# Optimization experiments

Hardware: AMD Instinct MI355X
Metric: run time of the kernel (lower is better)

## Reference

```python
import jax, jax.numpy as jnp
import numpy as np

SELF_DIM = 6   # self_state_dim
HID = 50       # lstm_hidden_dim


def setup_inputs() -> dict:
    key = jax.random.key(0)
    ks = jax.random.split(key, 16)
    B, N, D = 8192, 64, 13  # batch, num humans, joint-state length

    def w(k, shape):
        # kaiming-ish init, stored as [in, out] so forward is x @ W + b
        return jax.random.normal(k, shape, jnp.float32) / jnp.sqrt(jnp.float32(shape[0]))

    z = lambda n: jnp.zeros((n,), jnp.float32)
    return {
        "state": jax.random.normal(ks[0], (B, N, D), jnp.float32),
        # mlp1: 13 -> 150 -> 100, last_relu=True
        "mlp1_w1": w(ks[1], (13, 150)),  "mlp1_b1": z(150),
        "mlp1_w2": w(ks[2], (150, 100)), "mlp1_b2": z(100),
        # attention: 200 -> 100 -> 100 -> 1 (no relu on last)
        "attn_w1": w(ks[3], (200, 100)), "attn_b1": z(100),
        "attn_w2": w(ks[4], (100, 100)), "attn_b2": z(100),
        "attn_w3": w(ks[5], (100, 1)),   "attn_b3": z(1),
        # LSTM(input=7, hidden=50), torch gate order i,f,g,o
        "lstm_wih": w(ks[6], (7, 4 * HID)),
        "lstm_whh": w(ks[7], (HID, 4 * HID)),
        "lstm_bih": z(4 * HID), "lstm_bhh": z(4 * HID),
        # mlp: 56 -> 150 -> 100 -> 100 -> 1
        "mlp_w1": w(ks[8], (SELF_DIM + HID, 150)), "mlp_b1": z(150),
        "mlp_w2": w(ks[9], (150, 100)),            "mlp_b2": z(100),
        "mlp_w3": w(ks[10], (100, 100)),           "mlp_b3": z(100),
        "mlp_w4": w(ks[11], (100, 1)),             "mlp_b4": z(1),
    }


def reference(state, mlp1_w1, mlp1_b1, mlp1_w2, mlp1_b2,
              attn_w1, attn_b1, attn_w2, attn_b2, attn_w3, attn_b3,
              lstm_wih, lstm_whh, lstm_bih, lstm_bhh,
              mlp_w1, mlp_b1, mlp_w2, mlp_b2, mlp_w3, mlp_b3, mlp_w4, mlp_b4):
    relu = jax.nn.relu
    B, N, D = state.shape
    self_state = state[:, 0, :SELF_DIM]      # [B, 6]
    human_state = state[:, :, SELF_DIM:]     # [B, N, 7]

    # mlp1 over all B*N per-human joint-state rows (last_relu=True)
    flat = state.reshape(B * N, D)
    m1 = relu(relu(flat @ mlp1_w1 + mlp1_b1) @ mlp1_w2 + mlp1_b2)   # [B*N, 100]

    # mean-pooled global state, broadcast back per human, concat, attention score
    gdim = m1.shape[-1]
    global_state = jnp.mean(m1.reshape(B, N, gdim), axis=1, keepdims=True)
    global_state = jnp.broadcast_to(global_state, (B, N, gdim)).reshape(B * N, gdim)
    a_in = jnp.concatenate([m1, global_state], axis=1)               # [B*N, 200]
    scores = (relu(relu(a_in @ attn_w1 + attn_b1) @ attn_w2 + attn_b2) @ attn_w3 + attn_b3)
    scores = scores.reshape(B, N)
    # NOTE: in the original torch code `scores` only feed `rerank_human_state`,
    # which is never consumed (dead code) -- the LSTM runs on the UNSORTED
    # human_state. We keep the score computation for fidelity; the per-sample
    # argsort/gather is dropped since it does not affect the output.

    # LSTM over the N humans (batch_first in torch, h0=c0=0)
    xs = jnp.transpose(human_state, (1, 0, 2))   # [N, B, 7]
    h0 = jnp.zeros((B, HID), state.dtype)

    def step(carry, x_t):
        h, c = carry
        gates = x_t @ lstm_wih + h @ lstm_whh + lstm_bih + lstm_bhh  # [B, 4H]
        i, f, g, o = jnp.split(gates, 4, axis=-1)
        c = jax.nn.sigmoid(f) * c + jax.nn.sigmoid(i) * jnp.tanh(g)
        h = jax.nn.sigmoid(o) * jnp.tanh(c)
        return (h, c), None

    (hn, _cn), _ = jax.lax.scan(step, (h0, h0), xs)

    # value head on [self_state, h_n]
    joint = jnp.concatenate([self_state, hn], axis=1)   # [B, 56]
    x = relu(joint @ mlp_w1 + mlp_b1)
    x = relu(x @ mlp_w2 + mlp_b2)
    x = relu(x @ mlp_w3 + mlp_b3)
    value = x @ mlp_w4 + mlp_b4                          # [B, 1]
    return value
```

## Files before the change

kernel.cpp:

```cpp
#include <hip/hip_runtime.h>

typedef __attribute__((ext_vector_type(8))) short short8;
typedef __attribute__((ext_vector_type(4))) float f32x4;
union frag_u { short8 v; unsigned short u[8]; };

__device__ __forceinline__ float bf2f(unsigned short b) {
  unsigned int u = ((unsigned int)b) << 16;
  float f; __builtin_memcpy(&f, &u, 4); return f;
}
__device__ __forceinline__ unsigned short f2bf(float f) {
  unsigned int u; __builtin_memcpy(&u, &f, 4);
  return (unsigned short)((u + 0x7FFFu + ((u >> 16) & 1u)) >> 16);
}
__device__ __forceinline__ unsigned short hi_of(float f) { return f2bf(f); }
__device__ __forceinline__ unsigned short lo_of(float f) {
  unsigned short h = f2bf(f); return f2bf(f - bf2f(h));
}
__device__ __forceinline__ float sigm(float x) {
  return __builtin_amdgcn_rcpf(1.f + __expf(-x));
}
__device__ __forceinline__ float tanh_(float x) {
  return 1.f - 2.f * __builtin_amdgcn_rcpf(1.f + __expf(2.f * x));
}

__global__ void detect_dtype_kernel(const unsigned short* s, int* flag) {
  if (threadIdx.x == 0 && blockIdx.x == 0) {
    int insane = 0;
    for (int i = 0; i < 64; ++i) {
      unsigned short v = s[2 * i];
      int e = (v >> 7) & 0xFF;
      if (e < 100 || e > 140) insane++;
    }
    *flag = (insane >= 16) ? 1 : 0;
  }
}

template <int AS, typename GetB, typename GetW>
__device__ __forceinline__ void mfma_layer(const unsigned short* sA, float* sG,
    int wave, int col, int quad, int kc_n, int ntiles, int N, GetB getb, GetW getw)
{
  for (int tile = wave; tile < ntiles; tile += 8) {
    int n = tile * 16 + col;
    float b = (n < N) ? getb(n) : 0.f;
    f32x4 acc = {b, b, b, b};
    for (int kc = 0; kc < kc_n; ++kc) {
      short8 a = *(const short8*)&sA[col * AS + kc * 32 + quad * 8];
      frag_u w;
      #pragma unroll
      for (int j = 0; j < 8; ++j) {
        int k = kc * 32 + quad * 8 + j;
        w.u[j] = (n < N) ? getw(k, n) : (unsigned short)0;
      }
      acc = __builtin_amdgcn_mfma_f32_16x16x32_bf16(a, w.v, acc, 0, 0, 0);
    }
    *(f32x4*)&sG[n * 20 + quad * 4] = acc;
  }
}

template <int AS, bool LO>
__device__ __forceinline__ void relu_fill(const float* sG, unsigned short* sA,
                                          int tid, int N, int loOff, int Kpad) {
  for (int idx = tid; idx < 16 * Kpad; idx += 512) {
    int m = idx & 15, n = idx >> 4;
    unsigned short v = 0;
    if (n < N) {
      v = f2bf(fmaxf(sG[n * 20 + m], 0.f));
    } else if (LO && n >= loOff && n < loOff + N) {
      float x = fmaxf(sG[(n - loOff) * 20 + m], 0.f);
      v = lo_of(x);
    }
    sA[m * AS + n] = v;
  }
}

template <bool F32>
__global__ __launch_bounds__(512, 4) void value_net_kernel(
    const void* state_, const void* wih_, const void* whh_,
    const void* bih_, const void* bhh_,
    const void* w1_, const void* b1_, const void* w2_, const void* b2_,
    const void* w3_, const void* b3_, const void* w4_, const void* b4_,
    void* out_, const int* flag)
{
  if (flag && *flag != (F32 ? 1 : 0)) return;

  constexpr int AS = F32 ? 328 : 168;
  constexpr int KC = F32 ? 6 : 4;

  __shared__ __align__(16) unsigned short sA[16 * AS];
  __shared__ __align__(16) float sG[208 * 20];

  const unsigned short* st16 = (const unsigned short*)state_;
  const float*          stf  = (const float*)state_;

  const int tid  = threadIdx.x;
  const int wave = tid >> 6;
  const int lane = tid & 63;
  const int col  = lane & 15;
  const int quad = lane >> 4;
  const int r0   = blockIdx.x * 16;

  {
    unsigned int* a32 = (unsigned int*)sA;
    constexpr int ZN = (16 * AS / 2 + 511) / 512;
    #pragma unroll
    for (int i = 0; i < ZN; ++i) {
      int idx = tid + i * 512;
      if (idx < 16 * AS / 2) a32[idx] = 0;
    }
  }

  auto W_lstm = [&](int k, int n) -> unsigned short {
    if constexpr (!F32) {
      const unsigned short* wih = (const unsigned short*)wih_;
      const unsigned short* whh = (const unsigned short*)whh_;
      if (k < 7)   return wih[k * 200 + n];
      if (k < 57)  return whh[(k - 7) * 200 + n];
      if (k < 107) return whh[(k - 57) * 200 + n];
      return (unsigned short)0;
    } else {
      const float* wih = (const float*)wih_;
      const float* whh = (const float*)whh_;
      if (k < 7)   return hi_of(wih[k * 200 + n]);
      if (k < 14)  return hi_of(wih[(k - 7) * 200 + n]);
      if (k < 21)  return lo_of(wih[(k - 14) * 200 + n]);
      if (k < 71)  return hi_of(whh[(k - 21) * 200 + n]);
      if (k < 121) return hi_of(whh[(k - 71) * 200 + n]);
      if (k < 171) return lo_of(whh[(k - 121) * 200 + n]);
      return (unsigned short)0;
    }
  };
  auto ldf = [&](const void* p, int i) -> float {
    if constexpr (F32) return ((const float*)p)[i];
    else               return bf2f(((const unsigned short*)p)[i]);
  };

  const int nmine = (wave < 5) ? 2 : 1;
  frag_u wf[2][KC];
  float  wb[2];
  #pragma unroll
  for (int i = 0; i < 2; ++i) {
    if (i >= nmine) continue;
    int n = (wave + 8 * i) * 16 + col;
    #pragma unroll
    for (int kc = 0; kc < KC; ++kc) {
      #pragma unroll
      for (int j = 0; j < 8; ++j) {
        int k = kc * 32 + quad * 8 + j;
        wf[i][kc].u[j] = (n < 200) ? W_lstm(k, n) : (unsigned short)0;
      }
    }
    wb[i] = (n < 200) ? (ldf(bih_, n) + ldf(bhh_, n)) : 0.f;
  }

  int im[2], iu[2]; bool iv[2];
  float c_[2] = {0.f, 0.f}, hf[2] = {0.f, 0.f};
  #pragma unroll
  for (int i = 0; i < 2; ++i) {
    int idx = tid + 512 * i;
    iv[i] = idx < 800; im[i] = idx & 15; iu[i] = idx >> 4;
  }
  const int  xm = tid / 7, xd = tid - (tid / 7) * 7;
  const bool isx = tid < 112;
  auto xgidx = [&](int t) -> size_t { return (size_t)(r0 + xm) * 832 + t * 13 + 6 + xd; };
  auto xwrite = [&](float fv, unsigned short bv) {
    if constexpr (!F32) { sA[xm * AS + xd] = bv; }
    else {
      unsigned short h = f2bf(fv);
      sA[xm * AS + xd] = h; sA[xm * AS + 14 + xd] = h;
      sA[xm * AS + 7 + xd] = f2bf(fv - bf2f(h));
    }
  };

  unsigned short xv16 = 0; float xvf = 0.f;

  __syncthreads();
  if (isx) {
    if constexpr (!F32) { xwrite(0.f, st16[xgidx(0)]); xv16 = st16[xgidx(1)]; }
    else                { xwrite(stf[xgidx(0)], 0);    xvf  = stf[xgidx(1)]; }
  }
  __syncthreads();

  for (int t = 0; t < 64; ++t) {
    short8 a[KC];
    #pragma unroll
    for (int kc = 0; kc < KC; ++kc)
      a[kc] = *(const short8*)&sA[col * AS + kc * 32 + quad * 8];
    #pragma unroll
    for (int i = 0; i < 2; ++i) {
      if (i < nmine) {
        float b = wb[i];
        f32x4 acc = {b, b, b, b};
        #pragma unroll
        for (int kc = 0; kc < KC; ++kc)
          acc = __builtin_amdgcn_mfma_f32_16x16x32_bf16(a[kc], wf[i][kc].v, acc, 0, 0, 0);
        int n = (wave + 8 * i) * 16 + col;
        *(f32x4*)&sG[n * 20 + quad * 4] = acc;
      }
    }
    __syncthreads();
    #pragma unroll
    for (int i = 0; i < 2; ++i) {
      if (iv[i]) {
        int m = im[i], u = iu[i];
        float gi = sG[u * 20 + m];
        float gf = sG[(50 + u) * 20 + m];
        float gg = sG[(100 + u) * 20 + m];
        float go = sG[(150 + u) * 20 + m];
        float cc = sigm(gf) * c_[i] + sigm(gi) * tanh_(gg);
        c_[i] = cc;
        float h = sigm(go) * tanh_(cc);
        if (t < 63) {
          unsigned short hb = f2bf(h);
          unsigned short hl = f2bf(h - bf2f(hb));
          if constexpr (!F32) { sA[m * AS + 7 + u] = hb; sA[m * AS + 57 + u] = hl; }
          else { sA[m * AS + 21 + u] = hb; sA[m * AS + 121 + u] = hb; sA[m * AS + 71 + u] = hl; }
        } else hf[i] = h;
      }
    }
    if (isx && t < 63) {
      if constexpr (!F32) xwrite(0.f, xv16); else xwrite(xvf, 0);
      if (t < 62) { if constexpr (!F32) xv16 = st16[xgidx(t + 2)]; else xvf = stf[xgidx(t + 2)]; }
    }
    __syncthreads();
  }

  {
    unsigned int* a32 = (unsigned int*)sA;
    constexpr int ZN = (16 * AS / 2 + 511) / 512;
    #pragma unroll
    for (int i = 0; i < ZN; ++i) {
      int idx = tid + i * 512;
      if (idx < 16 * AS / 2) a32[idx] = 0;
    }
  }
  __syncthreads();
  #pragma unroll
  for (int i = 0; i < 2; ++i) {
    if (iv[i]) {
      int m = im[i], u = iu[i];
      unsigned short hb = f2bf(hf[i]);
      unsigned short hl = f2bf(hf[i] - bf2f(hb));
      sA[m * AS + 6 + u] = hb;
      if constexpr (!F32) sA[m * AS + 56 + u] = hl; else sA[m * AS + 62 + u] = hl;
    }
  }
  if (tid < 96) {
    int m = tid / 6, d = tid - (tid / 6) * 6;
    if constexpr (!F32) sA[m * AS + d] = st16[(size_t)(r0 + m) * 832 + d];
    else {
      float f = stf[(size_t)(r0 + m) * 832 + d];
      sA[m * AS + d] = hi_of(f); sA[m * AS + 56 + d] = lo_of(f);
    }
  }
  __syncthreads();

  mfma_layer<AS>(sA, sG, wave, col, quad, 4, 10, 150,
    [&](int n) { return ldf(b1_, n); },
    [&](int k, int n) -> unsigned short {
      if constexpr (!F32) {
        const unsigned short* w1 = (const unsigned short*)w1_;
        if (k < 56)  return w1[k * 150 + n];
        if (k < 106) return w1[(k - 50) * 150 + n];
        return (unsigned short)0;
      } else {
        const float* w1 = (const float*)w1_;
        if (k < 56)  return hi_of(w1[k * 150 + n]);
        if (k < 112) return hi_of(w1[(k - 56) * 150 + n]);
        return (unsigned short)0;
      }
    });
  __syncthreads();
  if constexpr (!F32) relu_fill<AS, false>(sG, sA, tid, 150, 160, 160);
  else                relu_fill<AS, true >(sG, sA, tid, 150, 150, 320);
  __syncthreads();

  mfma_layer<AS>(sA, sG, wave, col, quad, F32 ? 10 : 5, 7, 100,
    [&](int n) { return ldf(b2_, n); },
    [&](int k, int n) -> unsigned short {
      if constexpr (!F32) {
        const unsigned short* w2 = (const unsigned short*)w2_;
        return (k < 150) ? w2[k * 100 + n] : (unsigned short)0;
      } else {
        const float* w2 = (const float*)w2_;
        if (k < 150) return hi_of(w2[k * 100 + n]);
        if (k < 300) return hi_of(w2[(k - 150) * 100 + n]);
        return (unsigned short)0;
      }
    });
  __syncthreads();
  if constexpr (!F32) relu_fill<AS, false>(sG, sA, tid, 100, 128, 128);
  else                relu_fill<AS, true >(sG, sA, tid, 100, 100, 224);
  __syncthreads();

  mfma_layer<AS>(sA, sG, wave, col, quad, F32 ? 7 : 4, 7, 100,
    [&](int n) { return ldf(b3_, n); },
    [&](int k, int n) -> unsigned short {
      if constexpr (!F32) {
        const unsigned short* w3 = (const unsigned short*)w3_;
        return (k < 100) ? w3[k * 100 + n] : (unsigned short)0;
      } else {
        const float* w3 = (const float*)w3_;
        if (k < 100) return hi_of(w3[k * 100 + n]);
        if (k < 200) return hi_of(w3[(k - 100) * 100 + n]);
        return (unsigned short)0;
      }
    });
  __syncthreads();

  if (tid < 256) {
    int m = tid >> 4, j0 = tid & 15;
    float s = 0.f;
    for (int j = j0; j < 100; j += 16)
      s += fmaxf(sG[j * 20 + m], 0.f) * ldf(w4_, j);
    s += __shfl_xor(s, 8); s += __shfl_xor(s, 4);
    s += __shfl_xor(s, 2); s += __shfl_xor(s, 1);
    if (j0 == 0) {
      float v = s + ldf(b4_, 0);
      if constexpr (!F32) ((unsigned short*)out_)[r0 + m] = f2bf(v);
      else                ((float*)out_)[r0 + m] = v;
    }
  }
}

extern "C" void kernel_launch(void* const* d_in, const int* in_sizes, int n_in,
                              void* d_out, int out_size, void* d_ws, size_t ws_size,
                              hipStream_t stream) {
  (void)in_sizes; (void)n_in; (void)out_size;
  const void* state = d_in[0];
  const void* wih = d_in[11]; const void* whh = d_in[12];
  const void* bih = d_in[13]; const void* bhh = d_in[14];
  const void* w1  = d_in[15]; const void* b1  = d_in[16];
  const void* w2  = d_in[17]; const void* b2  = d_in[18];
  const void* w3  = d_in[19]; const void* b3  = d_in[20];
  const void* w4  = d_in[21]; const void* b4  = d_in[22];

  if (ws_size >= sizeof(int)) {
    int* flag = (int*)d_ws;
    detect_dtype_kernel<<<dim3(1), dim3(64), 0, stream>>>(
        (const unsigned short*)state, flag);
    value_net_kernel<false><<<dim3(512), dim3(512), 0, stream>>>(
        state, wih, whh, bih, bhh, w1, b1, w2, b2, w3, b3, w4, b4, d_out, flag);
    value_net_kernel<true><<<dim3(512), dim3(512), 0, stream>>>(
        state, wih, whh, bih, bhh, w1, b1, w2, b2, w3, b3, w4, b4, d_out, flag);
  } else {
    value_net_kernel<false><<<dim3(512), dim3(512), 0, stream>>>(
        state, wih, whh, bih, bhh, w1, b1, w2, b2, w3, b3, w4, b4, d_out,
        (const int*)nullptr);
  }
}
```

Measured before the change: 243.8 us.

## Double block size so each LSTM gate tile and cell gets its own thread

Grows the workgroup from 512 to 1024 threads (16 waves). Each of the 13 gate tiles now belongs to one wave, each of the 800 LSTM cell updates to one thread, and the x-prefetch moves to a separate set of spare threads. This shortens the serial critical path of every recurrent timestep, which previously had some waves doing two MFMA tiles and threads doing two cell updates. In exchange the blocks are larger, which may lower per-CU occupancy and register budget, and three of the sixteen waves sit idle at each barrier during the gate MFMA phase.

```diff
diff --git a/kernel.cpp b/kernel.cpp
--- a/kernel.cpp
+++ b/kernel.cpp
@@ -39,7 +39,7 @@
 __device__ __forceinline__ void mfma_layer(const unsigned short* sA, float* sG,
     int wave, int col, int quad, int kc_n, int ntiles, int N, GetB getb, GetW getw)
 {
-  for (int tile = wave; tile < ntiles; tile += 8) {
+  for (int tile = wave; tile < ntiles; tile += 16) {
     int n = tile * 16 + col;
     float b = (n < N) ? getb(n) : 0.f;
     f32x4 acc = {b, b, b, b};
@@ -60,7 +60,7 @@
 template <int AS, bool LO>
 __device__ __forceinline__ void relu_fill(const float* sG, unsigned short* sA,
                                           int tid, int N, int loOff, int Kpad) {
-  for (int idx = tid; idx < 16 * Kpad; idx += 512) {
+  for (int idx = tid; idx < 16 * Kpad; idx += 1024) {
     int m = idx & 15, n = idx >> 4;
     unsigned short v = 0;
     if (n < N) {
@@ -74,7 +74,7 @@
 }
 
 template <bool F32>
-__global__ __launch_bounds__(512, 4) void value_net_kernel(
+__global__ __launch_bounds__(1024, 8) void value_net_kernel(
     const void* state_, const void* wih_, const void* whh_,
     const void* bih_, const void* bhh_,
     const void* w1_, const void* b1_, const void* w2_, const void* b2_,
@@ -101,10 +101,10 @@
 
   {
     unsigned int* a32 = (unsigned int*)sA;
-    constexpr int ZN = (16 * AS / 2 + 511) / 512;
+    constexpr int ZN = (16 * AS / 2 + 1023) / 1024;
     #pragma unroll
     for (int i = 0; i < ZN; ++i) {
-      int idx = tid + i * 512;
+      int idx = tid + i * 1024;
       if (idx < 16 * AS / 2) a32[idx] = 0;
     }
   }
@@ -134,33 +134,28 @@
     else               return bf2f(((const unsigned short*)p)[i]);
   };
 
-  const int nmine = (wave < 5) ? 2 : 1;
-  frag_u wf[2][KC];
-  float  wb[2];
-  #pragma unroll
-  for (int i = 0; i < 2; ++i) {
-    if (i >= nmine) continue;
-    int n = (wave + 8 * i) * 16 + col;
+  const bool hasTile = (wave < 13);
+  frag_u wf[KC];
+  float  wb = 0.f;
+  if (hasTile) {
+    int n = wave * 16 + col;
     #pragma unroll
     for (int kc = 0; kc < KC; ++kc) {
       #pragma unroll
       for (int j = 0; j < 8; ++j) {
         int k = kc * 32 + quad * 8 + j;
-        wf[i][kc].u[j] = (n < 200) ? W_lstm(k, n) : (unsigned short)0;
-      }
-    }
-    wb[i] = (n < 200) ? (ldf(bih_, n) + ldf(bhh_, n)) : 0.f;
-  }
-
-  int im[2], iu[2]; bool iv[2];
-  float c_[2] = {0.f, 0.f}, hf[2] = {0.f, 0.f};
-  #pragma unroll
-  for (int i = 0; i < 2; ++i) {
-    int idx = tid + 512 * i;
-    iv[i] = idx < 800; im[i] = idx & 15; iu[i] = idx >> 4;
-  }
-  const int  xm = tid / 7, xd = tid - (tid / 7) * 7;
-  const bool isx = tid < 112;
+        wf[kc].u[j] = (n < 200) ? W_lstm(k, n) : (unsigned short)0;
+      }
+    }
+    wb = (n < 200) ? (ldf(bih_, n) + ldf(bhh_, n)) : 0.f;
+  }
+
+  const bool iv = tid < 800;
+  const int  im = tid & 15, iu = tid >> 4;
+  float c_ = 0.f, hf = 0.f;
+
+  const bool isx = (tid >= 800) && (tid < 912);
+  const int  xm = (tid - 800) / 7, xd = (tid - 800) - ((tid - 800) / 7) * 7;
   auto xgidx = [&](int t) -> size_t { return (size_t)(r0 + xm) * 832 + t * 13 + 6 + xd; };
   auto xwrite = [&](float fv, unsigned short bv) {
     if constexpr (!F32) { sA[xm * AS + xd] = bv; }
@@ -181,41 +176,33 @@
   __syncthreads();
 
   for (int t = 0; t < 64; ++t) {
-    short8 a[KC];
-    #pragma unroll
-    for (int kc = 0; kc < KC; ++kc)
-      a[kc] = *(const short8*)&sA[col * AS + kc * 32 + quad * 8];
-    #pragma unroll
-    for (int i = 0; i < 2; ++i) {
-      if (i < nmine) {
-        float b = wb[i];
-        f32x4 acc = {b, b, b, b};
-        #pragma unroll
-        for (int kc = 0; kc < KC; ++kc)
-          acc = __builtin_amdgcn_mfma_f32_16x16x32_bf16(a[kc], wf[i][kc].v, acc, 0, 0, 0);
-        int n = (wave + 8 * i) * 16 + col;
-        *(f32x4*)&sG[n * 20 + quad * 4] = acc;
-      }
+    if (hasTile) {
+      short8 a[KC];
+      #pragma unroll
+      for (int kc = 0; kc < KC; ++kc)
+        a[kc] = *(const short8*)&sA[col * AS + kc * 32 + quad * 8];
+      f32x4 acc = {wb, wb, wb, wb};
+      #pragma unroll
+      for (int kc = 0; kc < KC; ++kc)
+        acc = __builtin_amdgcn_mfma_f32_16x16x32_bf16(a[kc], wf[kc].v, acc, 0, 0, 0);
+      int n = wave * 16 + col;
+      *(f32x4*)&sG[n * 20 + quad * 4] = acc;
     }
     __syncthreads();
-    #pragma unroll
-    for (int i = 0; i < 2; ++i) {
-      if (iv[i]) {
-        int m = im[i], u = iu[i];
-        float gi = sG[u * 20 + m];
-        float gf = sG[(50 + u) * 20 + m];
-        float gg = sG[(100 + u) * 20 + m];
-        float go = sG[(150 + u) * 20 + m];
-        float cc = sigm(gf) * c_[i] + sigm(gi) * tanh_(gg);
-        c_[i] = cc;
-        float h = sigm(go) * tanh_(cc);
-        if (t < 63) {
-          unsigned short hb = f2bf(h);
-          unsigned short hl = f2bf(h - bf2f(hb));
-          if constexpr (!F32) { sA[m * AS + 7 + u] = hb; sA[m * AS + 57 + u] = hl; }
-          else { sA[m * AS + 21 + u] = hb; sA[m * AS + 121 + u] = hb; sA[m * AS + 71 + u] = hl; }
-        } else hf[i] = h;
-      }
+    if (iv) {
+      float gi = sG[iu * 20 + im];
+      float gf = sG[(50 + iu) * 20 + im];
+      float gg = sG[(100 + iu) * 20 + im];
+      float go = sG[(150 + iu) * 20 + im];
+      float cc = sigm(gf) * c_ + sigm(gi) * tanh_(gg);
+      c_ = cc;
+      float h = sigm(go) * tanh_(cc);
+      if (t < 63) {
+        unsigned short hb = f2bf(h);
+        unsigned short hl = f2bf(h - bf2f(hb));
+        if constexpr (!F32) { sA[im * AS + 7 + iu] = hb; sA[im * AS + 57 + iu] = hl; }
+        else { sA[im * AS + 21 + iu] = hb; sA[im * AS + 121 + iu] = hb; sA[im * AS + 71 + iu] = hl; }
+      } else hf = h;
     }
     if (isx && t < 63) {
       if constexpr (!F32) xwrite(0.f, xv16); else xwrite(xvf, 0);
@@ -226,23 +213,19 @@
 
   {
     unsigned int* a32 = (unsigned int*)sA;
-    constexpr int ZN = (16 * AS / 2 + 511) / 512;
+    constexpr int ZN = (16 * AS / 2 + 1023) / 1024;
     #pragma unroll
     for (int i = 0; i < ZN; ++i) {
-      int idx = tid + i * 512;
+      int idx = tid + i * 1024;
       if (idx < 16 * AS / 2) a32[idx] = 0;
     }
   }
   __syncthreads();
-  #pragma unroll
-  for (int i = 0; i < 2; ++i) {
-    if (iv[i]) {
-      int m = im[i], u = iu[i];
-      unsigned short hb = f2bf(hf[i]);
-      unsigned short hl = f2bf(hf[i] - bf2f(hb));
-      sA[m * AS + 6 + u] = hb;
-      if constexpr (!F32) sA[m * AS + 56 + u] = hl; else sA[m * AS + 62 + u] = hl;
-    }
+  if (iv) {
+    unsigned short hb = f2bf(hf);
+    unsigned short hl = f2bf(hf - bf2f(hb));
+    sA[im * AS + 6 + iu] = hb;
+    if constexpr (!F32) sA[im * AS + 56 + iu] = hl; else sA[im * AS + 62 + iu] = hl;
   }
   if (tid < 96) {
     int m = tid / 6, d = tid - (tid / 6) * 6;
@@ -338,12 +321,12 @@
     int* flag = (int*)d_ws;
     detect_dtype_kernel<<<dim3(1), dim3(64), 0, stream>>>(
         (const unsigned short*)state, flag);
-    value_net_kernel<false><<<dim3(512), dim3(512), 0, stream>>>(
+    value_net_kernel<false><<<dim3(512), dim3(1024), 0, stream>>>(
         state, wih, whh, bih, bhh, w1, b1, w2, b2, w3, b3, w4, b4, d_out, flag);
-    value_net_kernel<true><<<dim3(512), dim3(512), 0, stream>>>(
+    value_net_kernel<true><<<dim3(512), dim3(1024), 0, stream>>>(
         state, wih, whh, bih, bhh, w1, b1, w2, b2, w3, b3, w4, b4, d_out, flag);
   } else {
-    value_net_kernel<false><<<dim3(512), dim3(512), 0, stream>>>(
+    value_net_kernel<false><<<dim3(512), dim3(1024), 0, stream>>>(
         state, wih, whh, bih, bhh, w1, b1, w2, b2, w3, b3, w4, b4, d_out,
         (const int*)nullptr);
   }
```

Result: no change. 241.2 us (-1.1%).
